# Performance work log

Hardware: AMD Instinct MI355X
Metric: run time of the kernel (lower is better)

Reference implementation:

```python
import jax, jax.numpy as jnp
import numpy as np

D_MODEL = 64
LN_EPS = 1e-5


def _conv1d(x, w, b, stride, pad):
    # x: (B, Cin, L), w: (Cout, Cin, K)
    y = jax.lax.conv_general_dilated(x, w, (stride,), [(pad, pad)],
                                     dimension_numbers=('NCH', 'OIH', 'NCH'))
    return y + b[None, :, None]


def _layernorm(x, g, b):
    # normalize over last dim (feature dim), matching nn.LayerNorm(d_model)
    m = jnp.mean(x, axis=-1, keepdims=True)
    v = jnp.var(x, axis=-1, keepdims=True)
    return (x - m) * jax.lax.rsqrt(v + LN_EPS) * g + b


def _pos_embed(L, d):
    pos = jnp.arange(L, dtype=jnp.float32)[:, None]
    div = jnp.exp(jnp.arange(0, d, 2, dtype=jnp.float32) * (-np.log(10000.0) / d))
    pe = jnp.zeros((L, d), jnp.float32)
    pe = pe.at[:, 0::2].set(jnp.sin(pos * div))
    pe = pe.at[:, 1::2].set(jnp.cos(pos * div))
    return pe


def setup_inputs():
    key = jax.random.key(0)
    ks = jax.random.split(key, 20)
    B, L, D = 128, 4096, D_MODEL
    G = D // 4  # 16 convs per kernel-size group (kernels cycle [3,5,7,9])
    inp = {'x': jax.random.normal(ks[0], (B, 1, L), jnp.float32)}
    kernels = [3, 5, 7, 9]
    for i, k in enumerate(kernels):
        fan = float(1.0 / np.sqrt(k))
        inp['tok_w%d' % k] = jax.random.uniform(ks[1 + 2 * i], (G, 1, k), jnp.float32, -fan, fan)
        inp['tok_b%d' % k] = jax.random.uniform(ks[2 + 2 * i], (G,), jnp.float32, -fan, fan)
    fan = float(1.0 / np.sqrt(D * 4))
    for j in range(3):
        inp['c_w%d' % (j + 1)] = jax.random.uniform(ks[10 + 2 * j], (D, D, 4), jnp.float32, -fan, fan)
        inp['c_b%d' % (j + 1)] = jax.random.uniform(ks[11 + 2 * j], (D,), jnp.float32, -fan, fan)
    for j in range(2):
        inp['ln_g%d' % (j + 1)] = jnp.ones((D,), jnp.float32)
        inp['ln_b%d' % (j + 1)] = jnp.zeros((D,), jnp.float32)
    return inp


def reference(x, tok_w3, tok_b3, tok_w5, tok_b5, tok_w7, tok_b7, tok_w9, tok_b9,
              c_w1, c_b1, c_w2, c_b2, c_w3, c_b3, ln_g1, ln_b1, ln_g2, ln_b2):
    B, _, L = x.shape
    D = D_MODEL
    # TokenEmbedding: conv i has kernel [3,5,7,9][i%4]; fuse the d_model 1-channel
    # convs into 4 grouped convs (one per kernel size), then interleave channels.
    outs = [
        _conv1d(x, tok_w3, tok_b3, 1, 1),
        _conv1d(x, tok_w5, tok_b5, 1, 2),
        _conv1d(x, tok_w7, tok_b7, 1, 3),
        _conv1d(x, tok_w9, tok_b9, 1, 4),
    ]  # each (B, D//4, L); group g holds channels i with i % 4 == g, ordered by i // 4
    emb = jnp.stack(outs, axis=2).reshape(B, D, L)  # channel i = (i//4)*4 + (i%4)
    # add sinusoidal positional embedding (dropout is identity in eval mode)
    h = emb + _pos_embed(L, D).T[None]  # (B, D, L)
    # CompressionEmbedding: conv(k=4, s=2, p=1) -> tanh -> LN (over D) chain
    h = jnp.tanh(_conv1d(h, c_w1, c_b1, 2, 1))
    h = _layernorm(h.transpose(0, 2, 1), ln_g1, ln_b1).transpose(0, 2, 1)
    h = jnp.tanh(_conv1d(h, c_w2, c_b2, 2, 1))
    h = _layernorm(h.transpose(0, 2, 1), ln_g2, ln_b2).transpose(0, 2, 1)
    h = jnp.tanh(_conv1d(h, c_w3, c_b3, 2, 1))
    return h.transpose(0, 2, 1)  # (B, L//8, D)
```

## Files before the change

kernel.cpp:

```cpp
#include <hip/hip_runtime.h>
#include <math.h>

#define BATCH 128
#define LN_EPS 1e-5f

typedef short bf16x8 __attribute__((ext_vector_type(8)));
typedef short bf16x4 __attribute__((ext_vector_type(4)));
typedef float f32x4  __attribute__((ext_vector_type(4)));

__device__ __forceinline__ ushort f2bf(float f) {
    return __builtin_bit_cast(ushort, (__bf16)f);
}

__device__ __forceinline__ float fast_tanh(float v) {
    float e = __expf(2.f * v);
    return 1.f - 2.f / (e + 1.f);
}

__global__ __launch_bounds__(256, 2)
void prep_kernel(const float* __restrict__ cw1, const float* __restrict__ cw2,
                 const float* __restrict__ cw3,
                 const float* __restrict__ w3, const float* __restrict__ b3,
                 const float* __restrict__ w5, const float* __restrict__ b5,
                 const float* __restrict__ w7, const float* __restrict__ b7,
                 const float* __restrict__ w9, const float* __restrict__ b9,
                 const float* __restrict__ cb1, const float* __restrict__ cb2,
                 const float* __restrict__ cb3,
                 const float* __restrict__ lg1, const float* __restrict__ lb1,
                 const float* __restrict__ lg2, const float* __restrict__ lb2,
                 ushort* __restrict__ Wm23, ushort* __restrict__ Wm1,
                 float* __restrict__ W0c, float* __restrict__ W3c,
                 float* __restrict__ pe1c,
                 float* __restrict__ cb2t, float* __restrict__ B2k0,
                 float* __restrict__ B2k3,
                 float* __restrict__ cb3t, float* __restrict__ B3k0,
                 float* __restrict__ B3k3) {
    const int tid = threadIdx.x;
    const int bx  = blockIdx.x;
    const int idx = bx * 256 + tid;

    __shared__ float tile[64][132];
    __shared__ float red[4][64][24];
    __shared__ float cbred[64][4];

    {
        int s = idx >> 14, r = idx & 16383;
        int j = r & 7, l15 = (r >> 3) & 15, dt = (r >> 7) & 3;
        int quad = (r >> 9) & 3, k2 = (r >> 11) & 1, kk = (r >> 12) & 3;
        int dout = dt * 16 + l15, din = k2 * 32 + quad * 8 + j;
        const float* cw = (s == 0) ? cw2 : cw3;
        const float* lg = (s == 0) ? lg1 : lg2;
        Wm23[idx] = f2bf(cw[dout * 256 + din * 4 + kk] * lg[din]);
    }

    if (bx == 1 && tid < 128) {
        const int s = tid >> 6, ch = tid & 63;
        const float* cw = (s == 0) ? cw2 : cw3;
        const float* lb = (s == 0) ? lb1 : lb2;
        float full = 0.f, k0 = 0.f, k3 = 0.f;
        for (int din = 0; din < 64; ++din) {
            float bv = lb[din];
            const float* wr = cw + ch * 256 + din * 4;
            k0 = fmaf(wr[0], bv, k0);
            k3 = fmaf(wr[3], bv, k3);
            full = fmaf(wr[0] + wr[1] + wr[2] + wr[3], bv, full);
        }
        if (s == 0) { cb2t[ch] = cb2[ch] + full; B2k0[ch] = k0; B2k3[ch] = k3; }
        else        { cb3t[ch] = cb3[ch] + full; B3k0[ch] = k0; B3k3[ch] = k3; }
    }

    if (bx == 0) {
        const int ch = tid & 63, part = tid >> 6;
        const float* cw1row = cw1 + ch * 256;
        float acc[24];
#pragma unroll
        for (int j = 0; j < 24; ++j) acc[j] = 0.f;
        for (int din = part * 16; din < part * 16 + 16; ++din) {
            int ki = din & 3, g = din >> 2;
            float wl[9];
#pragma unroll
            for (int j = 0; j < 9; ++j) wl[j] = 0.f;
            float bias;
            if (ki == 0)      { for (int j = 0; j < 3; ++j) wl[3 + j] = w3[g * 3 + j]; bias = b3[g]; }
            else if (ki == 1) { for (int j = 0; j < 5; ++j) wl[2 + j] = w5[g * 5 + j]; bias = b5[g]; }
            else if (ki == 2) { for (int j = 0; j < 7; ++j) wl[1 + j] = w7[g * 7 + j]; bias = b7[g]; }
            else              { for (int j = 0; j < 9; ++j) wl[j]     = w9[g * 9 + j]; bias = b9[g]; }
#pragma unroll
            for (int kk = 0; kk < 4; ++kk) {
                float c = cw1row[din * 4 + kk];
                acc[12 + kk] += c * bias;
#pragma unroll
                for (int u = 0; u < 9; ++u) acc[kk + u] += c * wl[u];
            }
            float c0 = cw1row[din * 4 + 0], c3 = cw1row[din * 4 + 3];
#pragma unroll
            for (int u = 0; u < 4; ++u) { acc[16 + u] += c0 * wl[5 + u]; acc[20 + u] += c3 * wl[u]; }
        }
#pragma unroll
        for (int j = 0; j < 24; ++j) red[part][ch][j] = acc[j];
    }

    {
        const int pair = tid & 63, part = tid >> 6;
        const int kk = pair >> 4, chl = pair & 15;
        const int ch = (bx & 3) * 16 + chl;
        float s = 0.f;
        for (int din = part * 16; din < part * 16 + 16; ++din) {
            int ki = din & 3, g = din >> 2;
            float bias = (ki == 0) ? b3[g] : (ki == 1) ? b5[g] : (ki == 2) ? b7[g] : b9[g];
            s += cw1[ch * 256 + din * 4 + kk] * bias;
        }
        cbred[pair][part] = s;
    }

    const int l0 = (bx >> 2) * 64;
    const int pin0 = 2 * l0 - 1;
    for (int i2 = tid; i2 < 64 * 130; i2 += 256) {
        int d = i2 / 130, pp = i2 - d * 130;
        int p = pin0 + pp;
        float v = 0.f;
        if (p >= 0 && p < 4096) {
            float dv = __expf((float)(d & ~1) * -0.14391156831212787f);
            float ang = (float)p * dv;
            v = (d & 1) ? __cosf(ang) : __sinf(ang);
        }
        tile[d][pp] = v;
    }
    __syncthreads();

    if (bx == 0 && tid < 64) {
        const int ch = tid;
        float w24[24];
#pragma unroll
        for (int j = 0; j < 24; ++j)
            w24[j] = red[0][ch][j] + red[1][ch][j] + red[2][ch][j] + red[3][ch][j];
        int dt = ch >> 4, l15 = ch & 15;
#pragma unroll
        for (int quad = 0; quad < 4; ++quad)
#pragma unroll
            for (int j = 0; j < 8; ++j) {
                int k = quad * 8 + j;
                Wm1[((quad * 4 + dt) * 16 + l15) * 8 + j] = f2bf(k < 12 ? w24[k] : 0.f);
            }
#pragma unroll
        for (int u = 0; u < 4; ++u) { W0c[ch * 4 + u] = w24[16 + u]; W3c[ch * 4 + u] = w24[20 + u]; }
    }

    const int lane = tid & 63, wv = tid >> 6;
    const int l = l0 + lane;
    const int chl0 = wv * 4;
    const int db = (bx & 3) * 16 + chl0;
    float a4[4];
#pragma unroll
    for (int j = 0; j < 4; ++j) {
        int chl = chl0 + j;
        float cbk0 = cbred[0 * 16 + chl][0] + cbred[0 * 16 + chl][1] + cbred[0 * 16 + chl][2] + cbred[0 * 16 + chl][3];
        float cbk1 = cbred[1 * 16 + chl][0] + cbred[1 * 16 + chl][1] + cbred[1 * 16 + chl][2] + cbred[1 * 16 + chl][3];
        float cbk2 = cbred[2 * 16 + chl][0] + cbred[2 * 16 + chl][1] + cbred[2 * 16 + chl][2] + cbred[2 * 16 + chl][3];
        float cbk3 = cbred[3 * 16 + chl][0] + cbred[3 * 16 + chl][1] + cbred[3 * 16 + chl][2] + cbred[3 * 16 + chl][3];
        float a = cb1[db + j] + cbk1 + cbk2;
        if (l > 0) a += cbk0;
        if (l < 2047) a += cbk3;
        a4[j] = a;
    }
    for (int din = 0; din < 64; ++din) {
        float v0 = tile[din][2 * lane + 0], v1 = tile[din][2 * lane + 1];
        float v2 = tile[din][2 * lane + 2], v3 = tile[din][2 * lane + 3];
        const float* wb = cw1 + din * 4;
#pragma unroll
        for (int j = 0; j < 4; ++j) {
            const float* wj = wb + (db + j) * 256;
            a4[j] = fmaf(v0, wj[0], fmaf(v1, wj[1], fmaf(v2, wj[2], fmaf(v3, wj[3], a4[j]))));
        }
    }
    *(float4*)(pe1c + (size_t)l * 64 + db) = make_float4(a4[0], a4[1], a4[2], a4[3]);
}

__global__ __launch_bounds__(256, 2)
void mega_kernel(const float* __restrict__ x,
                 const ushort* __restrict__ Wm1, const ushort* __restrict__ Wm23,
                 const float* __restrict__ pe1c,
                 const float* __restrict__ W0c, const float* __restrict__ W3c,
                 const float* __restrict__ cb2t, const float* __restrict__ B2k0,
                 const float* __restrict__ B2k3,
                 const float* __restrict__ cb3t, const float* __restrict__ B3k0,
                 const float* __restrict__ B3k3,
                 float* __restrict__ out) {
    const int b = blockIdx.y;
    const int g0 = blockIdx.x * 32;
    const int tid = threadIdx.x;

    __shared__ __align__(16) ushort xs[320];
    __shared__ __align__(16) ushort TE1[68][72];
    __shared__ __align__(16) ushort TO1[68][72];
    __shared__ __align__(16) ushort TE2[34][72];
    __shared__ __align__(16) ushort TO2[34][72];

    for (int i = tid; i < 320; i += 256) {
        int g = 8 * g0 - 11 + i;
        float v = (g >= 0 && g < 4096) ? x[b * 4096 + g] : 0.f;
        xs[i] = f2bf(v);
    }
    __syncthreads();

    const int wv = tid >> 6, lane = tid & 63;
    const int quad = lane >> 4, l15 = lane & 15;

    {
        bf16x8 afr1[4];
#pragma unroll
        for (int dt = 0; dt < 4; ++dt)
            afr1[dt] = *(const bf16x8*)&Wm1[((quad * 4 + dt) * 16 + l15) * 8];
        const int qstart = 4 * g0 - 3;
        for (int pass = wv; pass < 9; pass += 4) {
            const int m = pass * 16 + l15;
            const int q = qstart + m;
            const int qc = (q < 0) ? 0 : ((q > 2047) ? 2047 : q);
            f32x4 a1[4];
            const float* pb_ = pe1c + (size_t)qc * 64 + quad * 4;
#pragma unroll
            for (int dt = 0; dt < 4; ++dt) {
                float4 pv = *(const float4*)(pb_ + dt * 16);
                a1[dt][0] = pv.x; a1[dt][1] = pv.y; a1[dt][2] = pv.z; a1[dt][3] = pv.w;
            }
            union { bf16x8 v; unsigned u[4]; } tmp;
            const unsigned* p = (const unsigned*)&xs[2 * m + 8 * quad];
#pragma unroll
            for (int i = 0; i < 4; ++i) tmp.u[i] = p[i];
#pragma unroll
            for (int dt = 0; dt < 4; ++dt)
                a1[dt] = __builtin_amdgcn_mfma_f32_16x16x32_bf16(
                    afr1[dt], tmp.v, a1[dt], 0, 0, 0);
            if (m < 134) {
                ushort* dst = (m & 1) ? &TE1[(m + 1) >> 1][0] : &TO1[m >> 1][0];
                if (q >= 0 && q < 2048) {
                    if (q == 0 || q == 2047) {
                        const float* Wc = (q == 0) ? W0c : W3c;
                        const float* xe = x + b * 4096 + ((q == 0) ? 0 : 4092);
                        float x0 = xe[0], x1 = xe[1], x2 = xe[2], x3 = xe[3];
#pragma unroll
                        for (int dt = 0; dt < 4; ++dt)
#pragma unroll
                            for (int r = 0; r < 4; ++r) {
                                const float* wc = Wc + (dt * 16 + quad * 4 + r) * 4;
                                a1[dt][r] -= wc[0] * x0 + wc[1] * x1 + wc[2] * x2 + wc[3] * x3;
                            }
                    }
                    float v[16], s = 0.f, s2 = 0.f;
#pragma unroll
                    for (int dt = 0; dt < 4; ++dt)
#pragma unroll
                        for (int r = 0; r < 4; ++r) {
                            float t = fast_tanh(a1[dt][r]);
                            v[dt * 4 + r] = t;
                            s += t;
                            s2 = fmaf(t, t, s2);
                        }
                    s += __shfl_xor(s, 16, 64);
                    s += __shfl_xor(s, 32, 64);
                    s2 += __shfl_xor(s2, 16, 64);
                    s2 += __shfl_xor(s2, 32, 64);
                    float mean = s * 0.015625f;
                    float var = fmaf(-mean, mean, s2 * 0.015625f);
                    float rstd = rsqrtf(var + LN_EPS);
                    float nmr = -mean * rstd;
#pragma unroll
                    for (int dt = 0; dt < 4; ++dt) {
                        bf16x4 pk;
#pragma unroll
                        for (int r = 0; r < 4; ++r)
                            pk[r] = (short)f2bf(fmaf(v[dt * 4 + r], rstd, nmr));
                        *(bf16x4*)(dst + dt * 16 + quad * 4) = pk;
                    }
                } else {
                    bf16x4 z; z[0] = 0; z[1] = 0; z[2] = 0; z[3] = 0;
#pragma unroll
                    for (int dt = 0; dt < 4; ++dt)
                        *(bf16x4*)(dst + dt * 16 + quad * 4) = z;
                }
            }
        }
    }
    __syncthreads();

    {
        f32x4 cfr2[4];
#pragma unroll
        for (int dt = 0; dt < 4; ++dt) {
            float4 cv = *(const float4*)(cb2t + dt * 16 + quad * 4);
            cfr2[dt][0] = cv.x; cfr2[dt][1] = cv.y; cfr2[dt][2] = cv.z; cfr2[dt][3] = cv.w;
        }
        for (int pass = wv; pass < 5; pass += 4) {
            const int n = pass * 16 + l15;
            const int nc = (n < 66) ? n : 65;
            f32x4 a2[4];
#pragma unroll
            for (int dt = 0; dt < 4; ++dt) a2[dt] = cfr2[dt];
#pragma unroll
            for (int kk = 0; kk < 4; ++kk) {
                const ushort (*T)[72] = (kk & 1) ? TE1 : TO1;
                const int row = nc + ((kk + 1) >> 1);
#pragma unroll
                for (int k2 = 0; k2 < 2; ++k2) {
                    bf16x8 bfr = *(const bf16x8*)&T[row][k2 * 32 + quad * 8];
                    const ushort* wb = Wm23 + ((((kk * 2 + k2) * 4 + quad) * 4) * 16) * 8;
#pragma unroll
                    for (int dt = 0; dt < 4; ++dt) {
                        bf16x8 afr = *(const bf16x8*)(wb + ((size_t)(dt * 16 + l15)) * 8);
                        a2[dt] = __builtin_amdgcn_mfma_f32_16x16x32_bf16(afr, bfr, a2[dt], 0, 0, 0);
                    }
                }
            }
            if (n < 66) {
                const int p = 2 * g0 - 1 + n;
                ushort* dst = (n & 1) ? &TE2[(n + 1) >> 1][0] : &TO2[n >> 1][0];
                if (p >= 0 && p < 1024) {
                    if (p == 0 || p == 1023) {
                        const float* Bc = (p == 0) ? B2k0 : B2k3;
#pragma unroll
                        for (int dt = 0; dt < 4; ++dt)
#pragma unroll
                            for (int r = 0; r < 4; ++r)
                                a2[dt][r] -= Bc[dt * 16 + quad * 4 + r];
                    }
                    float v[16], s = 0.f, s2 = 0.f;
#pragma unroll
                    for (int dt = 0; dt < 4; ++dt)
#pragma unroll
                        for (int r = 0; r < 4; ++r) {
                            float t = fast_tanh(a2[dt][r]);
                            v[dt * 4 + r] = t;
                            s += t;
                            s2 = fmaf(t, t, s2);
                        }
                    s += __shfl_xor(s, 16, 64);
                    s += __shfl_xor(s, 32, 64);
                    s2 += __shfl_xor(s2, 16, 64);
                    s2 += __shfl_xor(s2, 32, 64);
                    float mean = s * 0.015625f;
                    float var = fmaf(-mean, mean, s2 * 0.015625f);
                    float rstd = rsqrtf(var + LN_EPS);
                    float nmr = -mean * rstd;
#pragma unroll
                    for (int dt = 0; dt < 4; ++dt) {
                        bf16x4 pk;
#pragma unroll
                        for (int r = 0; r < 4; ++r)
                            pk[r] = (short)f2bf(fmaf(v[dt * 4 + r], rstd, nmr));
                        *(bf16x4*)(dst + dt * 16 + quad * 4) = pk;
                    }
                } else {
                    bf16x4 z; z[0] = 0; z[1] = 0; z[2] = 0; z[3] = 0;
#pragma unroll
                    for (int dt = 0; dt < 4; ++dt)
                        *(bf16x4*)(dst + dt * 16 + quad * 4) = z;
                }
            }
        }
    }
    __syncthreads();

    {
        const int m3 = (wv & 1) * 16 + l15;
        const int dth = wv >> 1;
        f32x4 a3[2];
#pragma unroll
        for (int d2 = 0; d2 < 2; ++d2) {
            float4 cv = *(const float4*)(cb3t + (dth * 2 + d2) * 16 + quad * 4);
            a3[d2][0] = cv.x; a3[d2][1] = cv.y; a3[d2][2] = cv.z; a3[d2][3] = cv.w;
        }
        const ushort* Wg3 = Wm23 + 16384;
#pragma unroll
        for (int kk = 0; kk < 4; ++kk) {
            const ushort (*T)[72] = (kk & 1) ? TE2 : TO2;
            const int row = m3 + ((kk + 1) >> 1);
#pragma unroll
            for (int k2 = 0; k2 < 2; ++k2) {
                bf16x8 bfr = *(const bf16x8*)&T[row][k2 * 32 + quad * 8];
                const ushort* wb = Wg3 + ((((kk * 2 + k2) * 4 + quad) * 4) * 16) * 8;
#pragma unroll
                for (int d2 = 0; d2 < 2; ++d2) {
                    const int dt = dth * 2 + d2;
                    bf16x8 afr = *(const bf16x8*)(wb + ((size_t)(dt * 16 + l15)) * 8);
                    a3[d2] = __builtin_amdgcn_mfma_f32_16x16x32_bf16(afr, bfr, a3[d2], 0, 0, 0);
                }
            }
        }
        const int l = g0 + m3;
        if (l == 0 || l == 511) {
            const float* Bc = (l == 0) ? B3k0 : B3k3;
#pragma unroll
            for (int d2 = 0; d2 < 2; ++d2)
#pragma unroll
                for (int r = 0; r < 4; ++r)
                    a3[d2][r] -= Bc[(dth * 2 + d2) * 16 + quad * 4 + r];
        }
        float* ob = out + ((size_t)(b * 512) + l) * 64;
#pragma unroll
        for (int d2 = 0; d2 < 2; ++d2) {
            const int dt = dth * 2 + d2;
            float4 st = make_float4(fast_tanh(a3[d2][0]),
                                    fast_tanh(a3[d2][1]),
                                    fast_tanh(a3[d2][2]),
                                    fast_tanh(a3[d2][3]));
            *(float4*)(ob + dt * 16 + quad * 4) = st;
        }
    }
}

extern "C" void kernel_launch(void* const* d_in, const int* in_sizes, int n_in,
                              void* d_out, int out_size, void* d_ws, size_t ws_size,
                              hipStream_t stream) {
    (void)in_sizes; (void)n_in; (void)out_size; (void)ws_size;
    const float* x   = (const float*)d_in[0];
    const float* w3  = (const float*)d_in[1];
    const float* b3  = (const float*)d_in[2];
    const float* w5  = (const float*)d_in[3];
    const float* b5  = (const float*)d_in[4];
    const float* w7  = (const float*)d_in[5];
    const float* b7  = (const float*)d_in[6];
    const float* w9  = (const float*)d_in[7];
    const float* b9  = (const float*)d_in[8];
    const float* cw1 = (const float*)d_in[9];
    const float* cb1 = (const float*)d_in[10];
    const float* cw2 = (const float*)d_in[11];
    const float* cb2 = (const float*)d_in[12];
    const float* cw3 = (const float*)d_in[13];
    const float* cb3 = (const float*)d_in[14];
    const float* lg1 = (const float*)d_in[15];
    const float* lb1 = (const float*)d_in[16];
    const float* lg2 = (const float*)d_in[17];
    const float* lb2 = (const float*)d_in[18];
    float* out = (float*)d_out;

    char* w = (char*)d_ws;
    ushort* Wm23 = (ushort*)(w + 0);
    ushort* Wm1  = (ushort*)(w + 65536);
    float*  W0c  = (float*)(w + 69632);
    float*  W3c  = (float*)(w + 70656);
    float*  cb2t = (float*)(w + 71680);
    float*  B2k0 = (float*)(w + 71936);
    float*  B2k3 = (float*)(w + 72192);
    float*  cb3t = (float*)(w + 72448);
    float*  B3k0 = (float*)(w + 72704);
    float*  B3k3 = (float*)(w + 72960);
    float*  pe1c = (float*)(w + 73216);

    prep_kernel<<<128, 256, 0, stream>>>(cw1, cw2, cw3, w3, b3, w5, b5, w7, b7, w9, b9,
                                         cb1, cb2, cb3, lg1, lb1, lg2, lb2,
                                         Wm23, Wm1, W0c, W3c, pe1c,
                                         cb2t, B2k0, B2k3, cb3t, B3k0, B3k3);
    mega_kernel<<<dim3(16, BATCH), 256, 0, stream>>>(
        x, Wm1, Wm23, pe1c, W0c, W3c, cb2t, B2k0, B2k3, cb3t, B3k0, B3k3, out);
}
```

Measured before the change: 163.5 us.

## Process two batch elements per block to reuse weight fragments and positional loads

Each block now handles batch elements b0 and b0+64, halving the grid in the batch dimension. Weight A-fragments, positional-embedding loads and bias setup are shared across the two batches, and the MFMA calls for both batches are interleaved to expose more independent work. The cost is doubled shared memory (about 58KB per block) and higher register pressure, which may cut occupancy below the launch-bounds target of two blocks per CU and reduces the total number of blocks.

```diff
diff --git a/kernel.cpp b/kernel.cpp
--- a/kernel.cpp
+++ b/kernel.cpp
@@ -186,20 +186,21 @@
                  const float* __restrict__ cb3t, const float* __restrict__ B3k0,
                  const float* __restrict__ B3k3,
                  float* __restrict__ out) {
-    const int b = blockIdx.y;
+    const int b0 = blockIdx.y;
     const int g0 = blockIdx.x * 32;
     const int tid = threadIdx.x;
 
-    __shared__ __align__(16) ushort xs[320];
-    __shared__ __align__(16) ushort TE1[68][72];
-    __shared__ __align__(16) ushort TO1[68][72];
-    __shared__ __align__(16) ushort TE2[34][72];
-    __shared__ __align__(16) ushort TO2[34][72];
-
-    for (int i = tid; i < 320; i += 256) {
-        int g = 8 * g0 - 11 + i;
-        float v = (g >= 0 && g < 4096) ? x[b * 4096 + g] : 0.f;
-        xs[i] = f2bf(v);
+    __shared__ __align__(16) ushort xs[2][320];
+    __shared__ __align__(16) ushort TE1[2][68][72];
+    __shared__ __align__(16) ushort TO1[2][68][72];
+    __shared__ __align__(16) ushort TE2[2][34][72];
+    __shared__ __align__(16) ushort TO2[2][34][72];
+
+    for (int i = tid; i < 640; i += 256) {
+        int ba = (i >= 320) ? 1 : 0, j = i - ba * 320;
+        int g = 8 * g0 - 11 + j;
+        float v = (g >= 0 && g < 4096) ? x[(size_t)(b0 + ba * 64) * 4096 + g] : 0.f;
+        xs[ba][j] = f2bf(v);
     }
     __syncthreads();
 
@@ -216,67 +217,79 @@
             const int m = pass * 16 + l15;
             const int q = qstart + m;
             const int qc = (q < 0) ? 0 : ((q > 2047) ? 2047 : q);
-            f32x4 a1[4];
             const float* pb_ = pe1c + (size_t)qc * 64 + quad * 4;
+            float4 pv[4];
+#pragma unroll
+            for (int dt = 0; dt < 4; ++dt) pv[dt] = *(const float4*)(pb_ + dt * 16);
+            union { bf16x8 v; unsigned u[4]; } tA, tB;
+            const unsigned* pA = (const unsigned*)&xs[0][2 * m + 8 * quad];
+            const unsigned* pB = (const unsigned*)&xs[1][2 * m + 8 * quad];
+#pragma unroll
+            for (int i = 0; i < 4; ++i) { tA.u[i] = pA[i]; tB.u[i] = pB[i]; }
+            f32x4 a1[2][4];
 #pragma unroll
             for (int dt = 0; dt < 4; ++dt) {
-                float4 pv = *(const float4*)(pb_ + dt * 16);
-                a1[dt][0] = pv.x; a1[dt][1] = pv.y; a1[dt][2] = pv.z; a1[dt][3] = pv.w;
-            }
-            union { bf16x8 v; unsigned u[4]; } tmp;
-            const unsigned* p = (const unsigned*)&xs[2 * m + 8 * quad];
-#pragma unroll
-            for (int i = 0; i < 4; ++i) tmp.u[i] = p[i];
-#pragma unroll
-            for (int dt = 0; dt < 4; ++dt)
-                a1[dt] = __builtin_amdgcn_mfma_f32_16x16x32_bf16(
-                    afr1[dt], tmp.v, a1[dt], 0, 0, 0);
+                f32x4 c;
+                c[0] = pv[dt].x; c[1] = pv[dt].y; c[2] = pv[dt].z; c[3] = pv[dt].w;
+                a1[0][dt] = __builtin_amdgcn_mfma_f32_16x16x32_bf16(afr1[dt], tA.v, c, 0, 0, 0);
+                a1[1][dt] = __builtin_amdgcn_mfma_f32_16x16x32_bf16(afr1[dt], tB.v, c, 0, 0, 0);
+            }
             if (m < 134) {
-                ushort* dst = (m & 1) ? &TE1[(m + 1) >> 1][0] : &TO1[m >> 1][0];
                 if (q >= 0 && q < 2048) {
-                    if (q == 0 || q == 2047) {
-                        const float* Wc = (q == 0) ? W0c : W3c;
-                        const float* xe = x + b * 4096 + ((q == 0) ? 0 : 4092);
-                        float x0 = xe[0], x1 = xe[1], x2 = xe[2], x3 = xe[3];
+#pragma unroll
+                    for (int ba = 0; ba < 2; ++ba) {
+                        ushort* dst = (m & 1) ? &TE1[ba][(m + 1) >> 1][0]
+                                              : &TO1[ba][m >> 1][0];
+                        if (q == 0 || q == 2047) {
+                            const float* Wc = (q == 0) ? W0c : W3c;
+                            const float* xe = x + (size_t)(b0 + ba * 64) * 4096
+                                                + ((q == 0) ? 0 : 4092);
+                            float x0 = xe[0], x1 = xe[1], x2 = xe[2], x3 = xe[3];
+#pragma unroll
+                            for (int dt = 0; dt < 4; ++dt)
+#pragma unroll
+                                for (int r = 0; r < 4; ++r) {
+                                    const float* wc = Wc + (dt * 16 + quad * 4 + r) * 4;
+                                    a1[ba][dt][r] -= wc[0] * x0 + wc[1] * x1 + wc[2] * x2 + wc[3] * x3;
+                                }
+                        }
+                        float v[16], s = 0.f, s2 = 0.f;
 #pragma unroll
                         for (int dt = 0; dt < 4; ++dt)
 #pragma unroll
                             for (int r = 0; r < 4; ++r) {
-                                const float* wc = Wc + (dt * 16 + quad * 4 + r) * 4;
-                                a1[dt][r] -= wc[0] * x0 + wc[1] * x1 + wc[2] * x2 + wc[3] * x3;
+                                float t = fast_tanh(a1[ba][dt][r]);
+                                v[dt * 4 + r] = t;
+                                s += t;
+                                s2 = fmaf(t, t, s2);
                             }
-                    }
-                    float v[16], s = 0.f, s2 = 0.f;
-#pragma unroll
-                    for (int dt = 0; dt < 4; ++dt)
-#pragma unroll
-                        for (int r = 0; r < 4; ++r) {
-                            float t = fast_tanh(a1[dt][r]);
-                            v[dt * 4 + r] = t;
-                            s += t;
-                            s2 = fmaf(t, t, s2);
+                        s += __shfl_xor(s, 16, 64);
+                        s += __shfl_xor(s, 32, 64);
+                        s2 += __shfl_xor(s2, 16, 64);
+                        s2 += __shfl_xor(s2, 32, 64);
+                        float mean = s * 0.015625f;
+                        float var = fmaf(-mean, mean, s2 * 0.015625f);
+                        float rstd = rsqrtf(var + LN_EPS);
+                        float nmr = -mean * rstd;
+#pragma unroll
+                        for (int dt = 0; dt < 4; ++dt) {
+                            bf16x4 pk;
+#pragma unroll
+                            for (int r = 0; r < 4; ++r)
+                                pk[r] = (short)f2bf(fmaf(v[dt * 4 + r], rstd, nmr));
+                            *(bf16x4*)(dst + dt * 16 + quad * 4) = pk;
                         }
-                    s += __shfl_xor(s, 16, 64);
-                    s += __shfl_xor(s, 32, 64);
-                    s2 += __shfl_xor(s2, 16, 64);
-                    s2 += __shfl_xor(s2, 32, 64);
-                    float mean = s * 0.015625f;
-                    float var = fmaf(-mean, mean, s2 * 0.015625f);
-                    float rstd = rsqrtf(var + LN_EPS);
-                    float nmr = -mean * rstd;
-#pragma unroll
-                    for (int dt = 0; dt < 4; ++dt) {
-                        bf16x4 pk;
-#pragma unroll
-                        for (int r = 0; r < 4; ++r)
-                            pk[r] = (short)f2bf(fmaf(v[dt * 4 + r], rstd, nmr));
-                        *(bf16x4*)(dst + dt * 16 + quad * 4) = pk;
                     }
                 } else {
                     bf16x4 z; z[0] = 0; z[1] = 0; z[2] = 0; z[3] = 0;
 #pragma unroll
-                    for (int dt = 0; dt < 4; ++dt)
-                        *(bf16x4*)(dst + dt * 16 + quad * 4) = z;
+                    for (int ba = 0; ba < 2; ++ba) {
+                        ushort* dst = (m & 1) ? &TE1[ba][(m + 1) >> 1][0]
+                                              : &TO1[ba][m >> 1][0];
+#pragma unroll
+                        for (int dt = 0; dt < 4; ++dt)
+                            *(bf16x4*)(dst + dt * 16 + quad * 4) = z;
+                    }
                 }
             }
         }
@@ -293,67 +306,79 @@
         for (int pass = wv; pass < 5; pass += 4) {
             const int n = pass * 16 + l15;
             const int nc = (n < 66) ? n : 65;
-            f32x4 a2[4];
-#pragma unroll
-            for (int dt = 0; dt < 4; ++dt) a2[dt] = cfr2[dt];
+            f32x4 a2[2][4];
+#pragma unroll
+            for (int dt = 0; dt < 4; ++dt) { a2[0][dt] = cfr2[dt]; a2[1][dt] = cfr2[dt]; }
 #pragma unroll
             for (int kk = 0; kk < 4; ++kk) {
-                const ushort (*T)[72] = (kk & 1) ? TE1 : TO1;
                 const int row = nc + ((kk + 1) >> 1);
 #pragma unroll
                 for (int k2 = 0; k2 < 2; ++k2) {
-                    bf16x8 bfr = *(const bf16x8*)&T[row][k2 * 32 + quad * 8];
+                    bf16x8 bfrA = (kk & 1) ? *(const bf16x8*)&TE1[0][row][k2 * 32 + quad * 8]
+                                           : *(const bf16x8*)&TO1[0][row][k2 * 32 + quad * 8];
+                    bf16x8 bfrB = (kk & 1) ? *(const bf16x8*)&TE1[1][row][k2 * 32 + quad * 8]
+                                           : *(const bf16x8*)&TO1[1][row][k2 * 32 + quad * 8];
                     const ushort* wb = Wm23 + ((((kk * 2 + k2) * 4 + quad) * 4) * 16) * 8;
 #pragma unroll
                     for (int dt = 0; dt < 4; ++dt) {
                         bf16x8 afr = *(const bf16x8*)(wb + ((size_t)(dt * 16 + l15)) * 8);
-                        a2[dt] = __builtin_amdgcn_mfma_f32_16x16x32_bf16(afr, bfr, a2[dt], 0, 0, 0);
+                        a2[0][dt] = __builtin_amdgcn_mfma_f32_16x16x32_bf16(afr, bfrA, a2[0][dt], 0, 0, 0);
+                        a2[1][dt] = __builtin_amdgcn_mfma_f32_16x16x32_bf16(afr, bfrB, a2[1][dt], 0, 0, 0);
                     }
                 }
             }
             if (n < 66) {
                 const int p = 2 * g0 - 1 + n;
-                ushort* dst = (n & 1) ? &TE2[(n + 1) >> 1][0] : &TO2[n >> 1][0];
                 if (p >= 0 && p < 1024) {
-                    if (p == 0 || p == 1023) {
-                        const float* Bc = (p == 0) ? B2k0 : B2k3;
+#pragma unroll
+                    for (int ba = 0; ba < 2; ++ba) {
+                        ushort* dst = (n & 1) ? &TE2[ba][(n + 1) >> 1][0]
+                                              : &TO2[ba][n >> 1][0];
+                        if (p == 0 || p == 1023) {
+                            const float* Bc = (p == 0) ? B2k0 : B2k3;
+#pragma unroll
+                            for (int dt = 0; dt < 4; ++dt)
+#pragma unroll
+                                for (int r = 0; r < 4; ++r)
+                                    a2[ba][dt][r] -= Bc[dt * 16 + quad * 4 + r];
+                        }
+                        float v[16], s = 0.f, s2 = 0.f;
 #pragma unroll
                         for (int dt = 0; dt < 4; ++dt)
 #pragma unroll
+                            for (int r = 0; r < 4; ++r) {
+                                float t = fast_tanh(a2[ba][dt][r]);
+                                v[dt * 4 + r] = t;
+                                s += t;
+                                s2 = fmaf(t, t, s2);
+                            }
+                        s += __shfl_xor(s, 16, 64);
+                        s += __shfl_xor(s, 32, 64);
+                        s2 += __shfl_xor(s2, 16, 64);
+                        s2 += __shfl_xor(s2, 32, 64);
+                        float mean = s * 0.015625f;
+                        float var = fmaf(-mean, mean, s2 * 0.015625f);
+                        float rstd = rsqrtf(var + LN_EPS);
+                        float nmr = -mean * rstd;
+#pragma unroll
+                        for (int dt = 0; dt < 4; ++dt) {
+                            bf16x4 pk;
+#pragma unroll
                             for (int r = 0; r < 4; ++r)
-                                a2[dt][r] -= Bc[dt * 16 + quad * 4 + r];
-                    }
-                    float v[16], s = 0.f, s2 = 0.f;
-#pragma unroll
-                    for (int dt = 0; dt < 4; ++dt)
-#pragma unroll
-                        for (int r = 0; r < 4; ++r) {
-                            float t = fast_tanh(a2[dt][r]);
-                            v[dt * 4 + r] = t;
-                            s += t;
-                            s2 = fmaf(t, t, s2);
+                                pk[r] = (short)f2bf(fmaf(v[dt * 4 + r], rstd, nmr));
+                            *(bf16x4*)(dst + dt * 16 + quad * 4) = pk;
                         }
-                    s += __shfl_xor(s, 16, 64);
-                    s += __shfl_xor(s, 32, 64);
-                    s2 += __shfl_xor(s2, 16, 64);
-                    s2 += __shfl_xor(s2, 32, 64);
-                    float mean = s * 0.015625f;
-                    float var = fmaf(-mean, mean, s2 * 0.015625f);
-                    float rstd = rsqrtf(var + LN_EPS);
-                    float nmr = -mean * rstd;
-#pragma unroll
-                    for (int dt = 0; dt < 4; ++dt) {
-                        bf16x4 pk;
-#pragma unroll
-                        for (int r = 0; r < 4; ++r)
-                            pk[r] = (short)f2bf(fmaf(v[dt * 4 + r], rstd, nmr));
-                        *(bf16x4*)(dst + dt * 16 + quad * 4) = pk;
                     }
                 } else {
                     bf16x4 z; z[0] = 0; z[1] = 0; z[2] = 0; z[3] = 0;
 #pragma unroll
-                    for (int dt = 0; dt < 4; ++dt)
-                        *(bf16x4*)(dst + dt * 16 + quad * 4) = z;
+                    for (int ba = 0; ba < 2; ++ba) {
+                        ushort* dst = (n & 1) ? &TE2[ba][(n + 1) >> 1][0]
+                                              : &TO2[ba][n >> 1][0];
+#pragma unroll
+                        for (int dt = 0; dt < 4; ++dt)
+                            *(bf16x4*)(dst + dt * 16 + quad * 4) = z;
+                    }
                 }
             }
         }
@@ -363,26 +388,30 @@
     {
         const int m3 = (wv & 1) * 16 + l15;
         const int dth = wv >> 1;
-        f32x4 a3[2];
+        f32x4 a3[2][2];
 #pragma unroll
         for (int d2 = 0; d2 < 2; ++d2) {
             float4 cv = *(const float4*)(cb3t + (dth * 2 + d2) * 16 + quad * 4);
-            a3[d2][0] = cv.x; a3[d2][1] = cv.y; a3[d2][2] = cv.z; a3[d2][3] = cv.w;
+            f32x4 c; c[0] = cv.x; c[1] = cv.y; c[2] = cv.z; c[3] = cv.w;
+            a3[0][d2] = c; a3[1][d2] = c;
         }
         const ushort* Wg3 = Wm23 + 16384;
 #pragma unroll
         for (int kk = 0; kk < 4; ++kk) {
-            const ushort (*T)[72] = (kk & 1) ? TE2 : TO2;
             const int row = m3 + ((kk + 1) >> 1);
 #pragma unroll
             for (int k2 = 0; k2 < 2; ++k2) {
-                bf16x8 bfr = *(const bf16x8*)&T[row][k2 * 32 + quad * 8];
+                bf16x8 bfrA = (kk & 1) ? *(const bf16x8*)&TE2[0][row][k2 * 32 + quad * 8]
+                                       : *(const bf16x8*)&TO2[0][row][k2 * 32 + quad * 8];
+                bf16x8 bfrB = (kk & 1) ? *(const bf16x8*)&TE2[1][row][k2 * 32 + quad * 8]
+                                       : *(const bf16x8*)&TO2[1][row][k2 * 32 + quad * 8];
                 const ushort* wb = Wg3 + ((((kk * 2 + k2) * 4 + quad) * 4) * 16) * 8;
 #pragma unroll
                 for (int d2 = 0; d2 < 2; ++d2) {
                     const int dt = dth * 2 + d2;
                     bf16x8 afr = *(const bf16x8*)(wb + ((size_t)(dt * 16 + l15)) * 8);
-                    a3[d2] = __builtin_amdgcn_mfma_f32_16x16x32_bf16(afr, bfr, a3[d2], 0, 0, 0);
+                    a3[0][d2] = __builtin_amdgcn_mfma_f32_16x16x32_bf16(afr, bfrA, a3[0][d2], 0, 0, 0);
+                    a3[1][d2] = __builtin_amdgcn_mfma_f32_16x16x32_bf16(afr, bfrB, a3[1][d2], 0, 0, 0);
                 }
             }
         }
@@ -390,20 +419,25 @@
         if (l == 0 || l == 511) {
             const float* Bc = (l == 0) ? B3k0 : B3k3;
 #pragma unroll
-            for (int d2 = 0; d2 < 2; ++d2)
-#pragma unroll
-                for (int r = 0; r < 4; ++r)
-                    a3[d2][r] -= Bc[(dth * 2 + d2) * 16 + quad * 4 + r];
-        }
-        float* ob = out + ((size_t)(b * 512) + l) * 64;
-#pragma unroll
-        for (int d2 = 0; d2 < 2; ++d2) {
-            const int dt = dth * 2 + d2;
-            float4 st = make_float4(fast_tanh(a3[d2][0]),
-                                    fast_tanh(a3[d2][1]),
-                                    fast_tanh(a3[d2][2]),
-                                    fast_tanh(a3[d2][3]));
-            *(float4*)(ob + dt * 16 + quad * 4) = st;
+            for (int ba = 0; ba < 2; ++ba)
+#pragma unroll
+                for (int d2 = 0; d2 < 2; ++d2)
+#pragma unroll
+                    for (int r = 0; r < 4; ++r)
+                        a3[ba][d2][r] -= Bc[(dth * 2 + d2) * 16 + quad * 4 + r];
+        }
+#pragma unroll
+        for (int ba = 0; ba < 2; ++ba) {
+            float* ob = out + ((size_t)((b0 + ba * 64) * 512) + l) * 64;
+#pragma unroll
+            for (int d2 = 0; d2 < 2; ++d2) {
+                const int dt = dth * 2 + d2;
+                float4 st = make_float4(fast_tanh(a3[ba][d2][0]),
+                                        fast_tanh(a3[ba][d2][1]),
+                                        fast_tanh(a3[ba][d2][2]),
+                                        fast_tanh(a3[ba][d2][3]));
+                *(float4*)(ob + dt * 16 + quad * 4) = st;
+            }
         }
     }
 }
@@ -450,6 +484,6 @@
                                          cb1, cb2, cb3, lg1, lb1, lg2, lb2,
                                          Wm23, Wm1, W0c, W3c, pe1c,
                                          cb2t, B2k0, B2k3, cb3t, B3k0, B3k3);
-    mega_kernel<<<dim3(16, BATCH), 256, 0, stream>>>(
+    mega_kernel<<<dim3(16, BATCH / 2), 256, 0, stream>>>(
         x, Wm1, Wm23, pe1c, W0c, W3c, cb2t, B2k0, B2k3, cb3t, B3k0, B3k3, out);
 }
```

Measured after the change: 154.9 us. 1.06x faster.
